# Optimization experiments

Hardware: AMD Instinct MI355X
Metric: run time of the kernel (lower is better)

Reference implementation:

```python
import jax, jax.numpy as jnp
import numpy as np

EPSILON = 1.0
SIGMA = 1.0
CUTOFF = 5.0
SHIFT = 4.0 * EPSILON * ((SIGMA / CUTOFF) ** 12 - (SIGMA / CUTOFF) ** 6)

N_ATOMS = 100000
N_EDGES = 6400000


def setup_inputs() -> dict:
    key = jax.random.key(0)
    k1, k2, k3 = jax.random.split(key, 3)
    distances = jax.random.normal(k1, (N_EDGES, 3), dtype=jnp.float32)
    first_atom = jax.random.randint(k2, (N_EDGES,), 0, N_ATOMS, dtype=jnp.int64)
    second_atom = jax.random.randint(k3, (N_EDGES,), 0, N_ATOMS, dtype=jnp.int64)
    return {
        "distances": distances,
        "first_atom": first_atom,
        "second_atom": second_atom,
        "n_atoms": N_ATOMS,
    }


def reference(distances, first_atom, second_atom, n_atoms):
    # per-edge LJ energy: r = |d|, e = 4*eps*((sigma/r)^12 - (sigma/r)^6) - shift
    r = jnp.linalg.norm(distances, axis=1)  # [E]
    sr6 = (SIGMA / r) ** 6
    sr12 = sr6 * sr6
    e = 4.0 * EPSILON * (sr12 - sr6) - SHIFT  # [E]
    # half-list: each edge contributes e/2 to both endpoints
    half_e = 0.5 * e
    energy = jax.ops.segment_sum(half_e, first_atom, num_segments=n_atoms)
    energy = energy + jax.ops.segment_sum(half_e, second_atom, num_segments=n_atoms)
    return energy  # [n_atoms] per-atom energies
```

## Files before the change

kernel.cpp:

```cpp
#include <hip/hip_runtime.h>

__device__ __constant__ float kShift = 4.0f * (float)(1.0 / 244140625.0 - 1.0 / 15625.0);

#define GROUPS 4
#define MEMBERS 64
#define BUCKET 25600
#define BLOCK_T 1024

__device__ __forceinline__ float lj_half_e(float x, float y, float z) {
    float r2 = x * x + y * y + z * z;
    float inv_r2 = 1.0f / r2;
    float sr6 = inv_r2 * inv_r2 * inv_r2;
    float sr12 = sr6 * sr6;
    float e = 4.0f * (sr12 - sr6) - kShift;
    return 0.5f * e;
}

__global__ __launch_bounds__(BLOCK_T) void lj_gather_group(
        const float* __restrict__ dist,
        const int* __restrict__ atom_a,
        const int* __restrict__ atom_b,
        float* __restrict__ ws,
        int n_atoms, int n_edges) {
    __shared__ float acc[BUCKET];

    const int g = blockIdx.x / MEMBERS;
    const int m = blockIdx.x % MEMBERS;
    const unsigned lo = (unsigned)(g * BUCKET);

    for (int i = threadIdx.x; i < BUCKET; i += BLOCK_T) acc[i] = 0.0f;
    __syncthreads();

    const long long quads = ((long long)n_edges + 3) / 4;
    const long long per = (quads + MEMBERS - 1) / MEMBERS;
    const long long q0 = (long long)m * per;
    const long long q1 = (q0 + per < quads) ? (q0 + per) : quads;

    for (long long q = q0 + threadIdx.x; q < q1; q += BLOCK_T) {
        long long e0 = q * 4;
        if (e0 + 3 < n_edges) {
            const float4* d4 = (const float4*)(dist) + (size_t)q * 3;
            float4 v0 = d4[0];
            float4 v1 = d4[1];
            float4 v2 = d4[2];
            int4 ia = ((const int4*)atom_a)[q];
            int4 ib = ((const int4*)atom_b)[q];

            float h0 = lj_half_e(v0.x, v0.y, v0.z);
            float h1 = lj_half_e(v0.w, v1.x, v1.y);
            float h2 = lj_half_e(v1.z, v1.w, v2.x);
            float h3 = lj_half_e(v2.y, v2.z, v2.w);

            unsigned r;
            r = (unsigned)ia.x - lo; if (r < BUCKET) atomicAdd(&acc[r], h0);
            r = (unsigned)ib.x - lo; if (r < BUCKET) atomicAdd(&acc[r], h0);
            r = (unsigned)ia.y - lo; if (r < BUCKET) atomicAdd(&acc[r], h1);
            r = (unsigned)ib.y - lo; if (r < BUCKET) atomicAdd(&acc[r], h1);
            r = (unsigned)ia.z - lo; if (r < BUCKET) atomicAdd(&acc[r], h2);
            r = (unsigned)ib.z - lo; if (r < BUCKET) atomicAdd(&acc[r], h2);
            r = (unsigned)ia.w - lo; if (r < BUCKET) atomicAdd(&acc[r], h3);
            r = (unsigned)ib.w - lo; if (r < BUCKET) atomicAdd(&acc[r], h3);
        } else {
            for (long long e = e0; e < n_edges; ++e) {
                float x = dist[e * 3 + 0];
                float y = dist[e * 3 + 1];
                float z = dist[e * 3 + 2];
                float h = lj_half_e(x, y, z);
                unsigned r;
                r = (unsigned)atom_a[e] - lo; if (r < BUCKET) atomicAdd(&acc[r], h);
                r = (unsigned)atom_b[e] - lo; if (r < BUCKET) atomicAdd(&acc[r], h);
            }
        }
    }
    __syncthreads();

    float* dst = ws + (size_t)blockIdx.x * BUCKET;
    for (int i = threadIdx.x; i < BUCKET; i += BLOCK_T) dst[i] = acc[i];
}

__global__ void reduce_groups(const float* __restrict__ ws,
                              float* __restrict__ out,
                              int n_atoms) {
    int i = blockIdx.x * blockDim.x + threadIdx.x;
    if (i >= n_atoms) return;
    int g = i / BUCKET;
    int off = i - g * BUCKET;
    const float* base = ws + ((size_t)g * MEMBERS) * BUCKET + off;
    float s = 0.0f;
    #pragma unroll 8
    for (int b = 0; b < MEMBERS; ++b) s += base[(size_t)b * BUCKET];
    out[i] = s;
}

__global__ void lj_scatter_direct(const float* __restrict__ dist,
                                  const int* __restrict__ atom_a,
                                  const int* __restrict__ atom_b,
                                  float* __restrict__ out,
                                  int n_edges) {
    int t = blockIdx.x * blockDim.x + threadIdx.x;
    long long e0 = (long long)t * 4;
    if (e0 >= n_edges) return;
    if (e0 + 3 < n_edges) {
        const float4* d4 = (const float4*)(dist) + (size_t)t * 3;
        float4 v0 = d4[0];
        float4 v1 = d4[1];
        float4 v2 = d4[2];
        int4 ia = ((const int4*)atom_a)[t];
        int4 ib = ((const int4*)atom_b)[t];
        float h0 = lj_half_e(v0.x, v0.y, v0.z);
        float h1 = lj_half_e(v0.w, v1.x, v1.y);
        float h2 = lj_half_e(v1.z, v1.w, v2.x);
        float h3 = lj_half_e(v2.y, v2.z, v2.w);
        atomicAdd(&out[ia.x], h0);
        atomicAdd(&out[ib.x], h0);
        atomicAdd(&out[ia.y], h1);
        atomicAdd(&out[ib.y], h1);
        atomicAdd(&out[ia.z], h2);
        atomicAdd(&out[ib.z], h2);
        atomicAdd(&out[ia.w], h3);
        atomicAdd(&out[ib.w], h3);
    } else {
        for (long long e = e0; e < n_edges; ++e) {
            float x = dist[e * 3 + 0];
            float y = dist[e * 3 + 1];
            float z = dist[e * 3 + 2];
            float h = lj_half_e(x, y, z);
            atomicAdd(&out[atom_a[e]], h);
            atomicAdd(&out[atom_b[e]], h);
        }
    }
}

extern "C" void kernel_launch(void* const* d_in, const int* in_sizes, int n_in,
                              void* d_out, int out_size, void* d_ws, size_t ws_size,
                              hipStream_t stream) {
    const float* dist = (const float*)d_in[0];
    const int* atom_a = (const int*)d_in[1];
    const int* atom_b = (const int*)d_in[2];
    float* out = (float*)d_out;

    int n_edges = in_sizes[1];
    int n_atoms = out_size;

    size_t need = (size_t)GROUPS * MEMBERS * BUCKET * sizeof(float);
    bool range_ok = ((long long)GROUPS * BUCKET >= (long long)n_atoms);

    if (ws_size >= need && range_ok) {
        float* ws = (float*)d_ws;
        lj_gather_group<<<GROUPS * MEMBERS, BLOCK_T, 0, stream>>>(
            dist, atom_a, atom_b, ws, n_atoms, n_edges);
        int rblock = 256;
        int rgrid = (n_atoms + rblock - 1) / rblock;
        reduce_groups<<<rgrid, rblock, 0, stream>>>(ws, out, n_atoms);
    } else {
        hipMemsetAsync(d_out, 0, (size_t)n_atoms * sizeof(float), stream);
        int n_quads = (n_edges + 3) / 4;
        int block = 256;
        int grid = (n_quads + block - 1) / block;
        lj_scatter_direct<<<grid, block, 0, stream>>>(dist, atom_a, atom_b, out, n_edges);
    }
}
```

Measured before the change: 202.5 us.

## Use three atom groups with 80 slices, interleaved block mapping, two-quad loads

Repartitions the shared-memory accumulation into 3 atom-range groups of about 33K atoms and 80 edge slices, giving 240 blocks instead of 256. Block indices are remapped so that blocks sharing an edge slice sit next to each other, which may improve L2/MALL reuse of the repeated edge reads. Each thread now loads two quads before computing, to raise memory-level parallelism. The tail handling moves out of the main loop, and the cost is a larger per-block LDS footprint and a reduction that sums 80 partials.

Result: no change. 201.3 us (-0.6%).

```diff
diff --git a/kernel.cpp b/kernel.cpp
--- a/kernel.cpp
+++ b/kernel.cpp
@@ -2,10 +2,11 @@
 
 __device__ __constant__ float kShift = 4.0f * (float)(1.0 / 244140625.0 - 1.0 / 15625.0);
 
-#define GROUPS 4
-#define MEMBERS 64
-#define BUCKET 25600
+#define GROUPS 3
+#define SLICES 80
+#define BUCKET 33334
 #define BLOCK_T 1024
+
 
 __device__ __forceinline__ float lj_half_e(float x, float y, float z) {
     float r2 = x * x + y * y + z * z;
@@ -21,60 +22,92 @@
         const int* __restrict__ atom_a,
         const int* __restrict__ atom_b,
         float* __restrict__ ws,
-        int n_atoms, int n_edges) {
+        int n_edges) {
     __shared__ float acc[BUCKET];
 
-    const int g = blockIdx.x / MEMBERS;
-    const int m = blockIdx.x % MEMBERS;
+    const int b = blockIdx.x;
+    const int r = b & 7;
+    const int t = b >> 3;
+    const int g = t % GROUPS;
+    const int k = t / GROUPS;
+    const int s = (k << 3) + r;
     const unsigned lo = (unsigned)(g * BUCKET);
 
     for (int i = threadIdx.x; i < BUCKET; i += BLOCK_T) acc[i] = 0.0f;
     __syncthreads();
 
-    const long long quads = ((long long)n_edges + 3) / 4;
-    const long long per = (quads + MEMBERS - 1) / MEMBERS;
-    const long long q0 = (long long)m * per;
-    const long long q1 = (q0 + per < quads) ? (q0 + per) : quads;
+    const long long quads = (long long)n_edges >> 2;
+    const long long per = (quads + SLICES - 1) / SLICES;
+    const long long q0 = (long long)s * per;
+    const long long qe = (q0 + per < quads) ? (q0 + per) : quads;
 
-    for (long long q = q0 + threadIdx.x; q < q1; q += BLOCK_T) {
-        long long e0 = q * 4;
-        if (e0 + 3 < n_edges) {
-            const float4* d4 = (const float4*)(dist) + (size_t)q * 3;
-            float4 v0 = d4[0];
-            float4 v1 = d4[1];
-            float4 v2 = d4[2];
-            int4 ia = ((const int4*)atom_a)[q];
-            int4 ib = ((const int4*)atom_b)[q];
+    for (long long base = q0; base < qe; base += 2 * BLOCK_T) {
+        long long qa = base + threadIdx.x;
+        long long qb = qa + BLOCK_T;
+        bool vA = (qa < qe);
+        bool vB = (qb < qe);
 
-            float h0 = lj_half_e(v0.x, v0.y, v0.z);
-            float h1 = lj_half_e(v0.w, v1.x, v1.y);
-            float h2 = lj_half_e(v1.z, v1.w, v2.x);
-            float h3 = lj_half_e(v2.y, v2.z, v2.w);
+        float4 A0, A1, A2, B0, B1, B2;
+        int4 IAa, IBa, IAb, IBb;
+        if (vA) {
+            const float4* d4 = (const float4*)(dist) + (size_t)qa * 3;
+            A0 = d4[0]; A1 = d4[1]; A2 = d4[2];
+            IAa = ((const int4*)atom_a)[qa];
+            IBa = ((const int4*)atom_b)[qa];
+        }
+        if (vB) {
+            const float4* d4 = (const float4*)(dist) + (size_t)qb * 3;
+            B0 = d4[0]; B1 = d4[1]; B2 = d4[2];
+            IAb = ((const int4*)atom_a)[qb];
+            IBb = ((const int4*)atom_b)[qb];
+        }
 
-            unsigned r;
-            r = (unsigned)ia.x - lo; if (r < BUCKET) atomicAdd(&acc[r], h0);
-            r = (unsigned)ib.x - lo; if (r < BUCKET) atomicAdd(&acc[r], h0);
-            r = (unsigned)ia.y - lo; if (r < BUCKET) atomicAdd(&acc[r], h1);
-            r = (unsigned)ib.y - lo; if (r < BUCKET) atomicAdd(&acc[r], h1);
-            r = (unsigned)ia.z - lo; if (r < BUCKET) atomicAdd(&acc[r], h2);
-            r = (unsigned)ib.z - lo; if (r < BUCKET) atomicAdd(&acc[r], h2);
-            r = (unsigned)ia.w - lo; if (r < BUCKET) atomicAdd(&acc[r], h3);
-            r = (unsigned)ib.w - lo; if (r < BUCKET) atomicAdd(&acc[r], h3);
-        } else {
-            for (long long e = e0; e < n_edges; ++e) {
-                float x = dist[e * 3 + 0];
-                float y = dist[e * 3 + 1];
-                float z = dist[e * 3 + 2];
-                float h = lj_half_e(x, y, z);
-                unsigned r;
-                r = (unsigned)atom_a[e] - lo; if (r < BUCKET) atomicAdd(&acc[r], h);
-                r = (unsigned)atom_b[e] - lo; if (r < BUCKET) atomicAdd(&acc[r], h);
-            }
+        if (vA) {
+            float h0 = lj_half_e(A0.x, A0.y, A0.z);
+            float h1 = lj_half_e(A0.w, A1.x, A1.y);
+            float h2 = lj_half_e(A1.z, A1.w, A2.x);
+            float h3 = lj_half_e(A2.y, A2.z, A2.w);
+            unsigned u;
+            u = (unsigned)IAa.x - lo; if (u < BUCKET) atomicAdd(&acc[u], h0);
+            u = (unsigned)IBa.x - lo; if (u < BUCKET) atomicAdd(&acc[u], h0);
+            u = (unsigned)IAa.y - lo; if (u < BUCKET) atomicAdd(&acc[u], h1);
+            u = (unsigned)IBa.y - lo; if (u < BUCKET) atomicAdd(&acc[u], h1);
+            u = (unsigned)IAa.z - lo; if (u < BUCKET) atomicAdd(&acc[u], h2);
+            u = (unsigned)IBa.z - lo; if (u < BUCKET) atomicAdd(&acc[u], h2);
+            u = (unsigned)IAa.w - lo; if (u < BUCKET) atomicAdd(&acc[u], h3);
+            u = (unsigned)IBa.w - lo; if (u < BUCKET) atomicAdd(&acc[u], h3);
+        }
+        if (vB) {
+            float h0 = lj_half_e(B0.x, B0.y, B0.z);
+            float h1 = lj_half_e(B0.w, B1.x, B1.y);
+            float h2 = lj_half_e(B1.z, B1.w, B2.x);
+            float h3 = lj_half_e(B2.y, B2.z, B2.w);
+            unsigned u;
+            u = (unsigned)IAb.x - lo; if (u < BUCKET) atomicAdd(&acc[u], h0);
+            u = (unsigned)IBb.x - lo; if (u < BUCKET) atomicAdd(&acc[u], h0);
+            u = (unsigned)IAb.y - lo; if (u < BUCKET) atomicAdd(&acc[u], h1);
+            u = (unsigned)IBb.y - lo; if (u < BUCKET) atomicAdd(&acc[u], h1);
+            u = (unsigned)IAb.z - lo; if (u < BUCKET) atomicAdd(&acc[u], h2);
+            u = (unsigned)IBb.z - lo; if (u < BUCKET) atomicAdd(&acc[u], h2);
+            u = (unsigned)IAb.w - lo; if (u < BUCKET) atomicAdd(&acc[u], h3);
+            u = (unsigned)IBb.w - lo; if (u < BUCKET) atomicAdd(&acc[u], h3);
+        }
+    }
+
+    if ((n_edges & 3) && s == SLICES - 1) {
+        for (long long e = quads * 4 + threadIdx.x; e < n_edges; e += BLOCK_T) {
+            float x = dist[e * 3 + 0];
+            float y = dist[e * 3 + 1];
+            float z = dist[e * 3 + 2];
+            float h = lj_half_e(x, y, z);
+            unsigned u;
+            u = (unsigned)atom_a[e] - lo; if (u < BUCKET) atomicAdd(&acc[u], h);
+            u = (unsigned)atom_b[e] - lo; if (u < BUCKET) atomicAdd(&acc[u], h);
         }
     }
     __syncthreads();
 
-    float* dst = ws + (size_t)blockIdx.x * BUCKET;
+    float* dst = ws + ((size_t)(g * SLICES + s)) * BUCKET;
     for (int i = threadIdx.x; i < BUCKET; i += BLOCK_T) dst[i] = acc[i];
 }
 
@@ -85,10 +118,10 @@
     if (i >= n_atoms) return;
     int g = i / BUCKET;
     int off = i - g * BUCKET;
-    const float* base = ws + ((size_t)g * MEMBERS) * BUCKET + off;
+    const float* base = ws + ((size_t)g * SLICES) * BUCKET + off;
     float s = 0.0f;
     #pragma unroll 8
-    for (int b = 0; b < MEMBERS; ++b) s += base[(size_t)b * BUCKET];
+    for (int b = 0; b < SLICES; ++b) s += base[(size_t)b * BUCKET];
     out[i] = s;
 }
 
@@ -142,13 +175,13 @@
     int n_edges = in_sizes[1];
     int n_atoms = out_size;
 
-    size_t need = (size_t)GROUPS * MEMBERS * BUCKET * sizeof(float);
+    size_t need = (size_t)GROUPS * SLICES * BUCKET * sizeof(float);
     bool range_ok = ((long long)GROUPS * BUCKET >= (long long)n_atoms);
 
     if (ws_size >= need && range_ok) {
         float* ws = (float*)d_ws;
-        lj_gather_group<<<GROUPS * MEMBERS, BLOCK_T, 0, stream>>>(
-            dist, atom_a, atom_b, ws, n_atoms, n_edges);
+        lj_gather_group<<<GROUPS * SLICES, BLOCK_T, 0, stream>>>(
+            dist, atom_a, atom_b, ws, n_edges);
         int rblock = 256;
         int rgrid = (n_atoms + rblock - 1) / rblock;
         reduce_groups<<<rgrid, rblock, 0, stream>>>(ws, out, n_atoms);
```
